# Optimization experiments

Hardware: AMD Instinct MI355X
Metric: run time of the kernel (lower is better)

## Reference

```python
import jax, jax.numpy as jnp
import numpy as np

BS, SL, WPL, NP = 32, 256, 4, 320
WD, PD, RD, HD = 768, 64, 64, 256
PN, RN, PL = 32, 64, 8
NF = 128
WINDOW_SIZES = (2, 3, 4)
FD = 2 * HD  # node feature dim


def setup_inputs() -> dict:
    key = jax.random.key(0)
    ks = jax.random.split(key, 24)
    s = 0.02
    inp = {}
    # forward tensors (bert_out stands in for BertModel output after CLS slice)
    inp["bert_out"] = jax.random.normal(ks[0], (BS, NP, WD), jnp.float32)
    inp["wordpiece_gather_idx"] = jax.random.randint(ks[1], (BS, SL, WPL), 0, NP + 1)
    inp["pos"] = jax.random.randint(ks[2], (BS, SL), 0, PN)
    inp["deprel"] = jax.random.randint(ks[3], (BS, SL), 0, RN)
    inp["path"] = jax.random.randint(ks[4], (BS, SL, PL), 0, 2 * SL + 1)
    inp["aspect_head"] = jax.random.randint(ks[5], (BS, SL), 0, SL + 1)
    inp["text_mask"] = jax.random.randint(ks[6], (BS, SL), 0, 2)
    inp["aspect_mask"] = jax.random.randint(ks[7], (BS, SL), 0, 2)
    # parameters (pad row 0 zeroed to mimic padding_idx)
    inp["pos_emb"] = (jax.random.normal(ks[8], (PN, PD)) * s).at[0].set(0.0)
    inp["deprel_emb"] = (jax.random.normal(ks[9], (RN, RD)) * s).at[0].set(0.0)
    inp["pathdepth_emb"] = (jax.random.normal(ks[10], (PL + 2, PD)) * s).at[0].set(0.0)
    inp["ext_rel"] = jax.random.normal(ks[11], (RD,)) * s
    inp["fc1_W"] = jax.random.normal(ks[12], (WD + 2 * PD, FD)) * s
    inp["fc1_b"] = jnp.zeros((FD,), jnp.float32)
    inp["bilin_W"] = jax.random.normal(ks[13], (2 * FD, RD)) * s
    inp["bilin_b"] = jnp.zeros((), jnp.float32)
    inp["W_k2"] = jax.random.normal(ks[14], (2, FD, NF)) * s
    inp["b_k2"] = jnp.zeros((NF,), jnp.float32)
    inp["W_k3"] = jax.random.normal(ks[15], (3, FD, NF)) * s
    inp["b_k3"] = jnp.zeros((NF,), jnp.float32)
    inp["W_k4"] = jax.random.normal(ks[16], (4, FD, NF)) * s
    inp["b_k4"] = jnp.zeros((NF,), jnp.float32)
    inp["fc_out_W"] = jax.random.normal(ks[17], (NF * 3, 3)) * s
    inp["fc_out_b"] = jnp.zeros((3,), jnp.float32)
    return inp


def reference(bert_out, wordpiece_gather_idx, pos, deprel, path, aspect_head,
              text_mask, aspect_mask, pos_emb, deprel_emb, pathdepth_emb, ext_rel,
              fc1_W, fc1_b, bilin_W, bilin_b,
              W_k2, b_k2, W_k3, b_k3, W_k4, b_k4, fc_out_W, fc_out_b):
    bs, sl = pos.shape
    wd = bert_out.shape[-1]
    fd = fc1_b.shape[0]
    # --- wordpiece -> word averaging (pad piece 0 is a zero vector) ---
    pieces = jnp.concatenate([jnp.zeros((bs, 1, wd), bert_out.dtype), bert_out], axis=1)  # [B, NP+1, WD]
    g = jnp.take_along_axis(pieces, wordpiece_gather_idx.reshape(bs, -1)[..., None], axis=1)
    g = g.reshape(bs, sl, -1, wd)                                   # [B, SL, WPL, WD]
    npieces = (wordpiece_gather_idx != 0).sum(-1, keepdims=True)    # [B, SL, 1]
    word = g.sum(2) / jnp.maximum(npieces, 1).astype(g.dtype)       # [B, SL, WD]
    # --- node features ---
    path_depth = (path != 0).sum(-1)                                # [B, SL]
    node_in = jnp.concatenate([word, pos_emb[pos], pathdepth_emb[path_depth]], -1)
    node = jax.nn.relu(node_in @ fc1_W + fc1_b)                     # [B, SL, FD]
    # --- edge features: gather head nodes (0 = pad word -> zeros) ---
    node_pad = jnp.concatenate([jnp.zeros((bs, 1, fd), node.dtype), node], axis=1)
    dep = jnp.take_along_axis(node_pad, aspect_head[..., None], axis=1)  # [B, SL, FD]
    head_text = jnp.concatenate([dep, node], axis=1)                # [B, 2SL, FD]
    tail_text = jnp.concatenate([node, jnp.zeros_like(node)], axis=1)
    edge = jnp.concatenate([head_text, tail_text], axis=-1)         # [B, 2SL, 2FD]
    label = jnp.concatenate([deprel_emb[deprel],
                             jnp.broadcast_to(ext_rel, (bs, sl, ext_rel.shape[0]))], axis=1)
    # bilinear score: x1^T W x2 + b, single output channel
    score = jax.nn.sigmoid(jnp.einsum('bnd,dr,bnr->bn', edge, bilin_W, label) + bilin_b)
    edge_score = jnp.concatenate([jnp.ones((bs, 1), score.dtype), score], axis=1)  # [B, 2SL+1]
    # --- node weight: product of edge scores along dependency path ---
    nw = jnp.prod(jnp.take_along_axis(edge_score[:, None, :], path, axis=2), -1)   # [B, SL]
    nw = jnp.where((text_mask != 0) & (aspect_mask == 0), nw, jnp.zeros_like(nw))
    weight_norm = nw.sum(-1)                                        # [B]
    # --- manual windowed CNN + max pool ---
    pooled = []
    for W, b in ((W_k2, b_k2), (W_k3, b_k3), (W_k4, b_k4)):
        kw = W.shape[0]
        cn = sl - kw + 1
        w_win = jnp.mean(jnp.stack([nw[:, k:k + cn] for k in range(kw)], -1), -1)  # [B, CN]
        y = sum(jnp.einsum('bnf,fm->bnm', node[:, k:k + cn, :], W[k]) for k in range(kw))
        y = w_win[..., None] * y + b                                # [B, CN, NF]
        pooled.append(y.max(axis=1))                                # [B, NF]
    sentence = jnp.concatenate(pooled, -1)
    predicts = sentence @ fc_out_W + fc_out_b                       # [B, 3]
    return predicts, weight_norm
```

## Files before the change

### kernel.cpp

```cpp
#include <hip/hip_runtime.h>
#include <hip/hip_bf16.h>
#include <math.h>

#define BSZ 32
#define SL 256
#define WPL 4
#define NP 320
#define WD 768
#define PD 64
#define RD 64
#define FD 512
#define PL 8
#define NF 128
#define NIN 896
#define ES_STRIDE 513
#define MROWS (BSZ * SL)
#define NZ 384
#define KZ 2048

typedef __attribute__((ext_vector_type(8))) short bf16x8;
typedef __attribute__((ext_vector_type(4))) float f32x4;
typedef unsigned short ushort_t;
typedef __attribute__((ext_vector_type(4))) ushort_t u16x4;

__device__ __forceinline__ ushort_t f2bf(float x) {
    __hip_bfloat16 h = __float2bfloat16(x);
    return *reinterpret_cast<ushort_t*>(&h);
}
__device__ __forceinline__ float bf2f(ushort_t u) {
    return __uint_as_float(((unsigned)u) << 16);
}

#define P0 65536
#define P1 (P0 + 512)
#define P2 (P1 + FD * NIN)
#define P3 (P2 + NZ * KZ)
#define P4 (P3 + 3 * FD)
#define PREP_BLOCKS (P4 / 256)
__global__ __launch_bounds__(256) void setup_kernel(
    const float* __restrict__ bert, const int* __restrict__ wgi,
    const int* __restrict__ pos, const int* __restrict__ path,
    const float* __restrict__ pos_emb, const float* __restrict__ pd_emb,
    const float* __restrict__ bilin_W, const float* __restrict__ deprel_emb,
    const float* __restrict__ ext_rel, const float* __restrict__ fc1_W,
    const float* __restrict__ W2, const float* __restrict__ W3,
    const float* __restrict__ W4,
    ushort_t* __restrict__ node_in,
    float* __restrict__ Ut, float* __restrict__ v,
    ushort_t* __restrict__ Wt1, ushort_t* __restrict__ WzT,
    ushort_t* __restrict__ node)
{
    const int tid = threadIdx.x;
    if (blockIdx.x < MROWS) {
        const int bs = blockIdx.x;
        const int b = bs >> 8;
        const int* gi = wgi + (size_t)bs * WPL;
        const int i0 = gi[0], i1 = gi[1], i2 = gi[2], i3 = gi[3];
        const int npc = (i0 != 0) + (i1 != 0) + (i2 != 0) + (i3 != 0);
        const float inv = 1.0f / (float)(npc > 1 ? npc : 1);
        ushort_t* out = node_in + (size_t)bs * NIN;
        if (tid < 192) {
            const float4* r0 = (const float4*)(bert + ((size_t)b * NP + (i0 - 1)) * WD);
            const float4* r1 = (const float4*)(bert + ((size_t)b * NP + (i1 - 1)) * WD);
            const float4* r2 = (const float4*)(bert + ((size_t)b * NP + (i2 - 1)) * WD);
            const float4* r3 = (const float4*)(bert + ((size_t)b * NP + (i3 - 1)) * WD);
            float4 s = make_float4(0.f, 0.f, 0.f, 0.f);
            if (i0) { float4 t = r0[tid]; s.x += t.x; s.y += t.y; s.z += t.z; s.w += t.w; }
            if (i1) { float4 t = r1[tid]; s.x += t.x; s.y += t.y; s.z += t.z; s.w += t.w; }
            if (i2) { float4 t = r2[tid]; s.x += t.x; s.y += t.y; s.z += t.z; s.w += t.w; }
            if (i3) { float4 t = r3[tid]; s.x += t.x; s.y += t.y; s.z += t.z; s.w += t.w; }
            u16x4 o;
            o[0] = f2bf(s.x * inv); o[1] = f2bf(s.y * inv);
            o[2] = f2bf(s.z * inv); o[3] = f2bf(s.w * inv);
            *reinterpret_cast<u16x4*>(&out[tid * 4]) = o;
        } else {
            const int e = tid - 192;
            out[WD + e] = f2bf(pos_emb[pos[bs] * PD + e]);
            const int* pp = path + (size_t)bs * PL;
            int pd = 0;
#pragma unroll
            for (int l = 0; l < PL; ++l) pd += (pp[l] != 0);
            out[WD + PD + e] = f2bf(pd_emb[pd * PD + e]);
        }
        return;
    }
    const int idx = (blockIdx.x - MROWS) * 256 + tid;
    if (idx < P0) {
        const int r = idx >> 10, d = idx & 1023;
        float s = 0.f;
#pragma unroll
        for (int j = 0; j < RD; ++j) s += bilin_W[d * RD + j] * deprel_emb[r * RD + j];
        Ut[idx] = s;
    } else if (idx < P1) {
        const int d = idx - P0;
        float s = 0.f;
#pragma unroll
        for (int j = 0; j < RD; ++j) s += bilin_W[d * RD + j] * ext_rel[j];
        v[d] = s;
    } else if (idx < P2) {
        const int j = idx - P1;
        const int k = j >> 9, n = j & 511;
        Wt1[(size_t)n * NIN + k] = f2bf(fc1_W[(size_t)k * FD + n]);
    } else if (idx < P3) {
        const int j = idx - P2;
        const int kp = j / NZ, c = j - kp * NZ;
        const int w = c >> 7, f = c & 127;
        const int k = kp >> 9, d = kp & 511;
        const int kw = w + 2;
        float val = 0.f;
        if (k < kw) {
            const float* Wsrc = (w == 0) ? W2 : (w == 1) ? W3 : W4;
            val = Wsrc[((size_t)k * FD + d) * NF + f];
        }
        WzT[(size_t)c * KZ + kp] = f2bf(val);
    } else if (idx < P4) {
        const int j = idx - P3;
        node[(size_t)MROWS * FD + j] = 0;
    }
}

__global__ __launch_bounds__(256) void gemm_node(
    const ushort_t* __restrict__ A,
    const ushort_t* __restrict__ Bt,
    const float* __restrict__ bias,
    ushort_t* __restrict__ C)
{
    __shared__ ushort_t As[128 * 64];
    __shared__ ushort_t Bs[64 * 64];
    const int tid = threadIdx.x;
    const int wid = tid >> 6, lane = tid & 63;
    const int wr = wid >> 1, wc = wid & 1;
    const int row0 = blockIdx.y * 128, col0 = blockIdx.x * 64;
    const int lr = lane & 15, lk = lane >> 4;
    f32x4 acc[4][2] = {};
    const ushort_t* gA0 = A + (size_t)row0 * NIN;
    const ushort_t* gB0 = Bt + (size_t)col0 * NIN;
    for (int k0 = 0; k0 < NIN; k0 += 64) {
#pragma unroll
        for (int i = 0; i < 4; ++i) {
            const int c = i * 256 + (wid << 6) + lane;
            const int r = c >> 3, q = (c & 7) ^ (r & 7);
            __builtin_amdgcn_global_load_lds(
                (const __attribute__((address_space(1))) void*)(gA0 + (size_t)r * NIN + k0 + q * 8),
                (__attribute__((address_space(3))) void*)((char*)As + i * 4096 + (wid << 10)),
                16, 0, 0);
        }
#pragma unroll
        for (int i = 0; i < 2; ++i) {
            const int c = i * 256 + (wid << 6) + lane;
            const int r = c >> 3, q = (c & 7) ^ (r & 7);
            __builtin_amdgcn_global_load_lds(
                (const __attribute__((address_space(1))) void*)(gB0 + (size_t)r * NIN + k0 + q * 8),
                (__attribute__((address_space(3))) void*)((char*)Bs + i * 4096 + (wid << 10)),
                16, 0, 0);
        }
        __syncthreads();
        bf16x8 af[4][2], bfv[2][2];
#pragma unroll
        for (int m = 0; m < 4; ++m) {
            const int fr = wr * 64 + m * 16 + lr;
#pragma unroll
            for (int ks = 0; ks < 2; ++ks)
                af[m][ks] = *reinterpret_cast<const bf16x8*>(
                    &As[fr * 64 + ((((ks << 2) | lk) ^ (fr & 7)) << 3)]);
        }
#pragma unroll
        for (int n = 0; n < 2; ++n) {
            const int fr = wc * 32 + n * 16 + lr;
#pragma unroll
            for (int ks = 0; ks < 2; ++ks)
                bfv[n][ks] = *reinterpret_cast<const bf16x8*>(
                    &Bs[fr * 64 + ((((ks << 2) | lk) ^ (fr & 7)) << 3)]);
        }
#pragma unroll
        for (int ks = 0; ks < 2; ++ks)
#pragma unroll
            for (int m = 0; m < 4; ++m)
#pragma unroll
                for (int n = 0; n < 2; ++n)
                    acc[m][n] = __builtin_amdgcn_mfma_f32_16x16x32_bf16(
                        af[m][ks], bfv[n][ks], acc[m][n], 0, 0, 0);
        __syncthreads();
    }
#pragma unroll
    for (int n = 0; n < 2; ++n) {
        const int col = col0 + wc * 32 + n * 16 + lr;
        const float bv = bias[col];
#pragma unroll
        for (int m = 0; m < 4; ++m) {
            const int rb = row0 + wr * 64 + m * 16 + lk * 4;
            const f32x4 vv = acc[m][n];
#pragma unroll
            for (int j = 0; j < 4; ++j)
                C[(size_t)(rb + j) * FD + col] = f2bf(fmaxf(vv[j] + bv, 0.f));
        }
    }
}

__global__ __launch_bounds__(256) void gemm_z_pool(
    const ushort_t* __restrict__ node,
    const ushort_t* __restrict__ WzT,
    const float* __restrict__ nw,
    const float* __restrict__ b2, const float* __restrict__ b3,
    const float* __restrict__ b4,
    float* __restrict__ pmaxp)
{
    __shared__ ushort_t As[128 * 64];
    __shared__ ushort_t Bs[64 * 64];
    const int tid = threadIdx.x;
    const int wid = tid >> 6, lane = tid & 63;
    const int wr = wid >> 1, wc = wid & 1;
    const int row0 = blockIdx.y * 128, col0 = blockIdx.x * 64;
    const int lr = lane & 15, lk = lane >> 4;
    f32x4 acc[4][2] = {};
    const ushort_t* gB0 = WzT + (size_t)col0 * KZ;
    const int Keff = ((col0 >> 7) + 2) * 512;
    for (int k0 = 0; k0 < Keff; k0 += 64) {
        const int koff = k0 >> 9;
        const int d0 = k0 & 511;
        const ushort_t* gA0 = node + (size_t)(row0 + koff) * FD + d0;
#pragma unroll
        for (int i = 0; i < 4; ++i) {
            const int c = i * 256 + (wid << 6) + lane;
            const int r = c >> 3, q = (c & 7) ^ (r & 7);
            __builtin_amdgcn_global_load_lds(
                (const __attribute__((address_space(1))) void*)(gA0 + (size_t)r * FD + q * 8),
                (__attribute__((address_space(3))) void*)((char*)As + i * 4096 + (wid << 10)),
                16, 0, 0);
        }
#pragma unroll
        for (int i = 0; i < 2; ++i) {
            const int c = i * 256 + (wid << 6) + lane;
            const int r = c >> 3, q = (c & 7) ^ (r & 7);
            __builtin_amdgcn_global_load_lds(
                (const __attribute__((address_space(1))) void*)(gB0 + (size_t)r * KZ + k0 + q * 8),
                (__attribute__((address_space(3))) void*)((char*)Bs + i * 4096 + (wid << 10)),
                16, 0, 0);
        }
        __syncthreads();
        bf16x8 af[4][2], bfv[2][2];
#pragma unroll
        for (int m = 0; m < 4; ++m) {
            const int fr = wr * 64 + m * 16 + lr;
#pragma unroll
            for (int ks = 0; ks < 2; ++ks)
                af[m][ks] = *reinterpret_cast<const bf16x8*>(
                    &As[fr * 64 + ((((ks << 2) | lk) ^ (fr & 7)) << 3)]);
        }
#pragma unroll
        for (int n = 0; n < 2; ++n) {
            const int fr = wc * 32 + n * 16 + lr;
#pragma unroll
            for (int ks = 0; ks < 2; ++ks)
                bfv[n][ks] = *reinterpret_cast<const bf16x8*>(
                    &Bs[fr * 64 + ((((ks << 2) | lk) ^ (fr & 7)) << 3)]);
        }
#pragma unroll
        for (int ks = 0; ks < 2; ++ks)
#pragma unroll
            for (int m = 0; m < 4; ++m)
#pragma unroll
                for (int n = 0; n < 2; ++n)
                    acc[m][n] = __builtin_amdgcn_mfma_f32_16x16x32_bf16(
                        af[m][ks], bfv[n][ks], acc[m][n], 0, 0, 0);
        __syncthreads();
    }
    const int bI = row0 >> 8;
    const int nn0 = row0 & 255;
    __shared__ float snw[132];
    if (tid < 132) snw[tid] = (nn0 + tid < SL) ? nw[bI * SL + nn0 + tid] : 0.f;
    __syncthreads();
    float cmax[2];
#pragma unroll
    for (int n = 0; n < 2; ++n) {
        const int col = col0 + wc * 32 + n * 16 + lr;
        const int w = col >> 7;
        const int kw = w + 2;
        const float invk = (w == 0) ? 0.5f : (w == 1) ? (1.f / 3.f) : 0.25f;
        const float bf = ((w == 0) ? b2 : (w == 1) ? b3 : b4)[col & 127];
        const int nmax = SL - kw;
        float mx = -INFINITY;
#pragma unroll
        for (int m = 0; m < 4; ++m) {
            const int rbase = wr * 64 + m * 16 + lk * 4;
            const f32x4 vv = acc[m][n];
#pragma unroll
            for (int j = 0; j < 4; ++j) {
                const int rloc = rbase + j;
                if (nn0 + rloc <= nmax) {
                    float ws = 0.f;
                    for (int k = 0; k < kw; ++k) ws += snw[rloc + k];
                    mx = fmaxf(mx, ws * invk * vv[j] + bf);
                }
            }
        }
        mx = fmaxf(mx, __shfl_xor(mx, 16));
        mx = fmaxf(mx, __shfl_xor(mx, 32));
        cmax[n] = mx;
    }
    if (lane < 16) {
#pragma unroll
        for (int n = 0; n < 2; ++n) {
            const int col = col0 + wc * 32 + n * 16 + lr;
            pmaxp[((size_t)blockIdx.y * 2 + wr) * NZ + col] = cmax[n];
        }
    }
}

__global__ __launch_bounds__(256) void score_kernel(
    const ushort_t* __restrict__ node, const int* __restrict__ aspect_head,
    const int* __restrict__ deprel, const float* __restrict__ Ut,
    const float* __restrict__ v, const float* __restrict__ bilin_b,
    float* __restrict__ edge_score)
{
    const int g = blockIdx.x * 4 + (threadIdx.x >> 6);
    const int lane = threadIdx.x & 63;
    const int b = g >> 9;
    const int n = g & 511;
    const int d0 = lane * 8;
    typedef __attribute__((ext_vector_type(8))) unsigned short u16x8;
    float sum = 0.f;
    if (n < SL) {
        const int dr = deprel[b * SL + n];
        const int h = aspect_head[b * SL + n];
        const float* uc = Ut + (size_t)dr * 1024;
        const u16x8 nv = *reinterpret_cast<const u16x8*>(&node[((size_t)b * SL + n) * FD + d0]);
        if (h != 0) {
            const u16x8 dv = *reinterpret_cast<const u16x8*>(&node[((size_t)b * SL + (h - 1)) * FD + d0]);
#pragma unroll
            for (int i = 0; i < 8; ++i) sum += bf2f(dv[i]) * uc[d0 + i];
        }
#pragma unroll
        for (int i = 0; i < 8; ++i) sum += bf2f(nv[i]) * uc[FD + d0 + i];
    } else {
        const u16x8 nv = *reinterpret_cast<const u16x8*>(&node[((size_t)b * SL + (n - SL)) * FD + d0]);
#pragma unroll
        for (int i = 0; i < 8; ++i) sum += bf2f(nv[i]) * v[d0 + i];
    }
#pragma unroll
    for (int off = 32; off > 0; off >>= 1) sum += __shfl_xor(sum, off, 64);
    if (lane == 0) {
        const float sc = 1.f / (1.f + expf(-(sum + bilin_b[0])));
        edge_score[b * ES_STRIDE + 1 + n] = sc;
        if (n == 0) edge_score[b * ES_STRIDE] = 1.0f;
    }
}

__global__ __launch_bounds__(256) void nw_kernel(
    const float* __restrict__ edge_score, const int* __restrict__ path,
    const int* __restrict__ text_mask, const int* __restrict__ aspect_mask,
    float* __restrict__ nw, float* __restrict__ weight_norm)
{
    const int b = blockIdx.x, s = threadIdx.x;
    const float* es = edge_score + b * ES_STRIDE;
    const int* pp = path + ((size_t)b * SL + s) * PL;
    float p = 1.f;
#pragma unroll
    for (int l = 0; l < PL; ++l) p *= es[pp[l]];
    if (!(text_mask[b * SL + s] != 0 && aspect_mask[b * SL + s] == 0)) p = 0.f;
    nw[b * SL + s] = p;
    __shared__ float red[256];
    red[s] = p;
    __syncthreads();
    for (int off = 128; off > 0; off >>= 1) {
        if (s < off) red[s] += red[s + off];
        __syncthreads();
    }
    if (s == 0) weight_norm[b] = red[0];
}

__global__ __launch_bounds__(384) void finish_kernel(
    const float* __restrict__ pmaxp, const float* __restrict__ W,
    const float* __restrict__ bias, float* __restrict__ out)
{
    const int b = blockIdx.x;
    const int t = threadIdx.x;
    const float* p = pmaxp + (size_t)b * 4 * NZ + t;
    float mx = -INFINITY;
#pragma unroll
    for (int i = 0; i < 4; ++i) mx = fmaxf(mx, p[(size_t)i * NZ]);
    __shared__ float sent[384];
    sent[t] = mx;
    __syncthreads();
    if (t < 3) {
        float acc = bias[t];
        for (int i = 0; i < 384; ++i) acc = fmaf(sent[i], W[i * 3 + t], acc);
        out[b * 3 + t] = acc;
    }
}

extern "C" void kernel_launch(void* const* d_in, const int* in_sizes, int n_in,
                              void* d_out, int out_size, void* d_ws, size_t ws_size,
                              hipStream_t stream)
{
    const float* bert      = (const float*)d_in[0];
    const int*   wgi       = (const int*)d_in[1];
    const int*   pos       = (const int*)d_in[2];
    const int*   deprel    = (const int*)d_in[3];
    const int*   path      = (const int*)d_in[4];
    const int*   ahead     = (const int*)d_in[5];
    const int*   tmask     = (const int*)d_in[6];
    const int*   amask     = (const int*)d_in[7];
    const float* pos_emb   = (const float*)d_in[8];
    const float* dre_emb   = (const float*)d_in[9];
    const float* pd_emb    = (const float*)d_in[10];
    const float* ext_rel   = (const float*)d_in[11];
    const float* fc1_W     = (const float*)d_in[12];
    const float* fc1_b     = (const float*)d_in[13];
    const float* bilin_W   = (const float*)d_in[14];
    const float* bilin_b   = (const float*)d_in[15];
    const float* W2        = (const float*)d_in[16];
    const float* b2        = (const float*)d_in[17];
    const float* W3        = (const float*)d_in[18];
    const float* b3        = (const float*)d_in[19];
    const float* W4        = (const float*)d_in[20];
    const float* b4        = (const float*)d_in[21];
    const float* fco_W     = (const float*)d_in[22];
    const float* fco_b     = (const float*)d_in[23];
    float* out = (float*)d_out;

    uint8_t* w = (uint8_t*)d_ws;
    ushort_t* node_in = (ushort_t*)w;
    size_t off = (size_t)MROWS * NIN * 2;
    ushort_t* node = (ushort_t*)(w + off); off += (size_t)(MROWS + 3) * FD * 2;
    ushort_t* Wt1  = (ushort_t*)(w + off); off += (size_t)FD * NIN * 2;
    ushort_t* WzT  = (ushort_t*)(w + off); off += (size_t)NZ * KZ * 2;
    float* Ut    = (float*)(w + off); off += (size_t)64 * 1024 * 4;
    float* vvec  = (float*)(w + off); off += FD * 4;
    float* es    = (float*)(w + off); off += (size_t)BSZ * ES_STRIDE * 4;
    float* nw    = (float*)(w + off); off += (size_t)BSZ * SL * 4;
    float* pmaxp = (float*)(w + off); off += (size_t)128 * NZ * 4;

    setup_kernel<<<MROWS + PREP_BLOCKS, 256, 0, stream>>>(
        bert, wgi, pos, path, pos_emb, pd_emb,
        bilin_W, dre_emb, ext_rel, fc1_W, W2, W3, W4,
        node_in, Ut, vvec, Wt1, WzT, node);

    gemm_node<<<dim3(FD / 64, MROWS / 128), 256, 0, stream>>>(node_in, Wt1, fc1_b, node);

    score_kernel<<<(BSZ * 2 * SL) / 4, 256, 0, stream>>>(
        node, ahead, deprel, Ut, vvec, bilin_b, es);

    nw_kernel<<<BSZ, 256, 0, stream>>>(es, path, tmask, amask, nw, out + 96);

    gemm_z_pool<<<dim3(NZ / 64, MROWS / 128), 256, 0, stream>>>(
        node, WzT, nw, b2, b3, b4, pmaxp);

    finish_kernel<<<BSZ, 384, 0, stream>>>(pmaxp, fco_W, fco_b, out);
}
```

Baseline: 112.3 us.

## Precompute embedding projections as bias tables and fuse score with node-weight kernel

The pos and path-depth embedding columns are no longer concatenated into the fc1 input. Their fc1 contributions, with fc1_b folded in, are precomputed into small tables (32 and 10 rows by 512) that the GEMM epilogue adds per row, so the GEMM K dimension drops from 896 to 768. Weight transposes now go through shared-memory 32x32 tiles, which gives coalesced writes. The score and nw kernels are merged into one 32-block kernel that keeps edge scores in LDS, removing a launch and a global round-trip, but this gives much less parallelism for the score computation. The epilogue also adds gathered bias loads per element.

Result: slower. 149.0 us (+32.7%).

```diff
diff --git a/kernel.cpp b/kernel.cpp
--- a/kernel.cpp
+++ b/kernel.cpp
@@ -12,7 +12,6 @@
 #define FD 512
 #define PL 8
 #define NF 128
-#define NIN 896
 #define ES_STRIDE 513
 #define MROWS (BSZ * SL)
 #define NZ 384
@@ -31,34 +30,42 @@
     return __uint_as_float(((unsigned)u) << 16);
 }
 
-#define P0 65536
-#define P1 (P0 + 512)
-#define P2 (P1 + FD * NIN)
-#define P3 (P2 + NZ * KZ)
-#define P4 (P3 + 3 * FD)
-#define PREP_BLOCKS (P4 / 256)
+#define NB_GATHER MROWS
+#define B_WW   NB_GATHER
+#define NB_WW  384
+#define B_TAB  (B_WW + NB_WW)
+#define NB_TAB 42
+#define B_WZT  (B_TAB + NB_TAB)
+#define NB_WZT 576
+#define B_PAD  (B_WZT + NB_WZT)
+#define NB_PAD 2
+#define B_UT   (B_PAD + NB_PAD)
+#define NB_UT  258
+#define NB_TOTAL (B_UT + NB_UT)
+
 __global__ __launch_bounds__(256) void setup_kernel(
     const float* __restrict__ bert, const int* __restrict__ wgi,
     const int* __restrict__ pos, const int* __restrict__ path,
     const float* __restrict__ pos_emb, const float* __restrict__ pd_emb,
     const float* __restrict__ bilin_W, const float* __restrict__ deprel_emb,
     const float* __restrict__ ext_rel, const float* __restrict__ fc1_W,
+    const float* __restrict__ fc1_b,
     const float* __restrict__ W2, const float* __restrict__ W3,
     const float* __restrict__ W4,
-    ushort_t* __restrict__ node_in,
-    float* __restrict__ Ut, float* __restrict__ v,
-    ushort_t* __restrict__ Wt1, ushort_t* __restrict__ WzT,
-    ushort_t* __restrict__ node)
+    ushort_t* __restrict__ word, int* __restrict__ depth,
+    ushort_t* __restrict__ Ww, float* __restrict__ posc, float* __restrict__ pdc,
+    ushort_t* __restrict__ WzT, ushort_t* __restrict__ node,
+    float* __restrict__ Ut, float* __restrict__ v)
 {
     const int tid = threadIdx.x;
-    if (blockIdx.x < MROWS) {
-        const int bs = blockIdx.x;
+    const int blk = blockIdx.x;
+    if (blk < NB_GATHER) {
+        const int bs = blk;
         const int b = bs >> 8;
         const int* gi = wgi + (size_t)bs * WPL;
         const int i0 = gi[0], i1 = gi[1], i2 = gi[2], i3 = gi[3];
         const int npc = (i0 != 0) + (i1 != 0) + (i2 != 0) + (i3 != 0);
         const float inv = 1.0f / (float)(npc > 1 ? npc : 1);
-        ushort_t* out = node_in + (size_t)bs * NIN;
         if (tid < 192) {
             const float4* r0 = (const float4*)(bert + ((size_t)b * NP + (i0 - 1)) * WD);
             const float4* r1 = (const float4*)(bert + ((size_t)b * NP + (i1 - 1)) * WD);
@@ -72,76 +79,132 @@
             u16x4 o;
             o[0] = f2bf(s.x * inv); o[1] = f2bf(s.y * inv);
             o[2] = f2bf(s.z * inv); o[3] = f2bf(s.w * inv);
-            *reinterpret_cast<u16x4*>(&out[tid * 4]) = o;
-        } else {
-            const int e = tid - 192;
-            out[WD + e] = f2bf(pos_emb[pos[bs] * PD + e]);
+            *reinterpret_cast<u16x4*>(&word[(size_t)bs * WD + tid * 4]) = o;
+        } else if (tid == 192) {
             const int* pp = path + (size_t)bs * PL;
             int pd = 0;
 #pragma unroll
             for (int l = 0; l < PL; ++l) pd += (pp[l] != 0);
-            out[WD + PD + e] = f2bf(pd_emb[pd * PD + e]);
+            depth[bs] = pd;
         }
         return;
     }
-    const int idx = (blockIdx.x - MROWS) * 256 + tid;
-    if (idx < P0) {
-        const int r = idx >> 10, d = idx & 1023;
-        float s = 0.f;
-#pragma unroll
-        for (int j = 0; j < RD; ++j) s += bilin_W[d * RD + j] * deprel_emb[r * RD + j];
-        Ut[idx] = s;
-    } else if (idx < P1) {
-        const int d = idx - P0;
-        float s = 0.f;
-#pragma unroll
-        for (int j = 0; j < RD; ++j) s += bilin_W[d * RD + j] * ext_rel[j];
-        v[d] = s;
-    } else if (idx < P2) {
-        const int j = idx - P1;
-        const int k = j >> 9, n = j & 511;
-        Wt1[(size_t)n * NIN + k] = f2bf(fc1_W[(size_t)k * FD + n]);
-    } else if (idx < P3) {
-        const int j = idx - P2;
-        const int kp = j / NZ, c = j - kp * NZ;
-        const int w = c >> 7, f = c & 127;
-        const int k = kp >> 9, d = kp & 511;
-        const int kw = w + 2;
-        float val = 0.f;
-        if (k < kw) {
-            const float* Wsrc = (w == 0) ? W2 : (w == 1) ? W3 : W4;
-            val = Wsrc[((size_t)k * FD + d) * NF + f];
-        }
-        WzT[(size_t)c * KZ + kp] = f2bf(val);
-    } else if (idx < P4) {
-        const int j = idx - P3;
-        node[(size_t)MROWS * FD + j] = 0;
+    if (blk < B_TAB) {
+        __shared__ float s[32][33];
+        const int t = blk - B_WW;
+        const int kt = t % 24, nt = t / 24;
+#pragma unroll
+        for (int i = 0; i < 4; ++i) {
+            const int idx = i * 256 + tid;
+            const int kk = idx >> 5, nn = idx & 31;
+            s[kk][nn] = fc1_W[(size_t)(kt * 32 + kk) * FD + nt * 32 + nn];
+        }
+        __syncthreads();
+#pragma unroll
+        for (int i = 0; i < 4; ++i) {
+            const int idx = i * 256 + tid;
+            const int nn = idx >> 5, kk = idx & 31;
+            Ww[(size_t)(nt * 32 + nn) * WD + kt * 32 + kk] = f2bf(s[kk][nn]);
+        }
+        return;
+    }
+    if (blk < B_WZT) {
+        const int r = blk - B_TAB;
+#pragma unroll
+        for (int h = 0; h < 2; ++h) {
+            const int cc = tid + h * 256;
+            if (r < 32) {
+                float acc = fc1_b[cc];
+#pragma unroll
+                for (int j = 0; j < PD; ++j)
+                    acc += pos_emb[r * PD + j] * fc1_W[(size_t)(WD + j) * FD + cc];
+                posc[(size_t)r * FD + cc] = acc;
+            } else {
+                const int r2 = r - 32;
+                float acc = 0.f;
+#pragma unroll
+                for (int j = 0; j < PD; ++j)
+                    acc += pd_emb[r2 * PD + j] * fc1_W[(size_t)(WD + PD + j) * FD + cc];
+                pdc[(size_t)r2 * FD + cc] = acc;
+            }
+        }
+        return;
+    }
+    if (blk < B_PAD) {
+        __shared__ float s[32][33];
+        const int t2 = blk - B_WZT;
+        const int p = t2 / 64, tt = t2 % 64;
+        const int dt = tt & 15, ft = tt >> 4;
+        int w, k; const float* src;
+        if (p < 2)      { w = 0; k = p;     src = W2; }
+        else if (p < 5) { w = 1; k = p - 2; src = W3; }
+        else            { w = 2; k = p - 5; src = W4; }
+#pragma unroll
+        for (int i = 0; i < 4; ++i) {
+            const int idx = i * 256 + tid;
+            const int dd = idx >> 5, ff = idx & 31;
+            s[dd][ff] = src[((size_t)k * FD + dt * 32 + dd) * NF + ft * 32 + ff];
+        }
+        __syncthreads();
+#pragma unroll
+        for (int i = 0; i < 4; ++i) {
+            const int idx = i * 256 + tid;
+            const int ff = idx >> 5, dd = idx & 31;
+            WzT[(size_t)(w * NF + ft * 32 + ff) * KZ + k * FD + dt * 32 + dd] = f2bf(s[dd][ff]);
+        }
+        return;
+    }
+    if (blk < B_UT) {
+        const int local = (blk - B_PAD) * 256 + tid;
+#pragma unroll
+        for (int j = 0; j < 3; ++j) node[(size_t)MROWS * FD + local * 3 + j] = 0;
+        return;
+    }
+    {
+        const int idx = (blk - B_UT) * 256 + tid;
+        if (idx < 65536) {
+            const int r = idx >> 10, d = idx & 1023;
+            float s = 0.f;
+#pragma unroll
+            for (int j = 0; j < RD; ++j) s += bilin_W[d * RD + j] * deprel_emb[r * RD + j];
+            Ut[idx] = s;
+        } else if (idx < 65536 + FD) {
+            const int d = idx - 65536;
+            float s = 0.f;
+#pragma unroll
+            for (int j = 0; j < RD; ++j) s += bilin_W[d * RD + j] * ext_rel[j];
+            v[d] = s;
+        }
+        return;
     }
 }
 
 __global__ __launch_bounds__(256) void gemm_node(
     const ushort_t* __restrict__ A,
     const ushort_t* __restrict__ Bt,
-    const float* __restrict__ bias,
+    const int* __restrict__ pos, const int* __restrict__ depth,
+    const float* __restrict__ posc, const float* __restrict__ pdc,
     ushort_t* __restrict__ C)
 {
     __shared__ ushort_t As[128 * 64];
     __shared__ ushort_t Bs[64 * 64];
+    __shared__ int spos[128], sdep[128];
     const int tid = threadIdx.x;
     const int wid = tid >> 6, lane = tid & 63;
     const int wr = wid >> 1, wc = wid & 1;
     const int row0 = blockIdx.y * 128, col0 = blockIdx.x * 64;
     const int lr = lane & 15, lk = lane >> 4;
+    if (tid < 128) { spos[tid] = pos[row0 + tid]; sdep[tid] = depth[row0 + tid]; }
     f32x4 acc[4][2] = {};
-    const ushort_t* gA0 = A + (size_t)row0 * NIN;
-    const ushort_t* gB0 = Bt + (size_t)col0 * NIN;
-    for (int k0 = 0; k0 < NIN; k0 += 64) {
+    const ushort_t* gA0 = A + (size_t)row0 * WD;
+    const ushort_t* gB0 = Bt + (size_t)col0 * WD;
+    for (int k0 = 0; k0 < WD; k0 += 64) {
 #pragma unroll
         for (int i = 0; i < 4; ++i) {
             const int c = i * 256 + (wid << 6) + lane;
             const int r = c >> 3, q = (c & 7) ^ (r & 7);
             __builtin_amdgcn_global_load_lds(
-                (const __attribute__((address_space(1))) void*)(gA0 + (size_t)r * NIN + k0 + q * 8),
+                (const __attribute__((address_space(1))) void*)(gA0 + (size_t)r * WD + k0 + q * 8),
                 (__attribute__((address_space(3))) void*)((char*)As + i * 4096 + (wid << 10)),
                 16, 0, 0);
         }
@@ -150,7 +213,7 @@
             const int c = i * 256 + (wid << 6) + lane;
             const int r = c >> 3, q = (c & 7) ^ (r & 7);
             __builtin_amdgcn_global_load_lds(
-                (const __attribute__((address_space(1))) void*)(gB0 + (size_t)r * NIN + k0 + q * 8),
+                (const __attribute__((address_space(1))) void*)(gB0 + (size_t)r * WD + k0 + q * 8),
                 (__attribute__((address_space(3))) void*)((char*)Bs + i * 4096 + (wid << 10)),
                 16, 0, 0);
         }
@@ -185,16 +248,77 @@
 #pragma unroll
     for (int n = 0; n < 2; ++n) {
         const int col = col0 + wc * 32 + n * 16 + lr;
-        const float bv = bias[col];
 #pragma unroll
         for (int m = 0; m < 4; ++m) {
-            const int rb = row0 + wr * 64 + m * 16 + lk * 4;
             const f32x4 vv = acc[m][n];
 #pragma unroll
-            for (int j = 0; j < 4; ++j)
-                C[(size_t)(rb + j) * FD + col] = f2bf(fmaxf(vv[j] + bv, 0.f));
-        }
-    }
+            for (int j = 0; j < 4; ++j) {
+                const int rloc = wr * 64 + m * 16 + lk * 4 + j;
+                const float bv = posc[(size_t)spos[rloc] * FD + col]
+                               + pdc[(size_t)sdep[rloc] * FD + col];
+                C[(size_t)(row0 + rloc) * FD + col] = f2bf(fmaxf(vv[j] + bv, 0.f));
+            }
+        }
+    }
+}
+
+__global__ __launch_bounds__(512) void score_nw_kernel(
+    const ushort_t* __restrict__ node, const int* __restrict__ aspect_head,
+    const int* __restrict__ deprel, const float* __restrict__ Ut,
+    const float* __restrict__ v, const float* __restrict__ bilin_b,
+    const int* __restrict__ path, const int* __restrict__ text_mask,
+    const int* __restrict__ aspect_mask,
+    float* __restrict__ nw, float* __restrict__ weight_norm)
+{
+    __shared__ float es[ES_STRIDE];
+    __shared__ float red[256];
+    const int b = blockIdx.x;
+    const int tid = threadIdx.x;
+    const int wv = tid >> 6, lane = tid & 63;
+    const int d0 = lane * 8;
+    const float bb = bilin_b[0];
+    typedef __attribute__((ext_vector_type(8))) unsigned short u16x8;
+    if (tid == 0) es[0] = 1.0f;
+    for (int e = wv; e < 2 * SL; e += 8) {
+        float sum = 0.f;
+        if (e < SL) {
+            const int dr = deprel[b * SL + e];
+            const int h = aspect_head[b * SL + e];
+            const float* uc = Ut + (size_t)dr * 1024;
+            const u16x8 nv = *reinterpret_cast<const u16x8*>(&node[((size_t)b * SL + e) * FD + d0]);
+            if (h != 0) {
+                const u16x8 dv = *reinterpret_cast<const u16x8*>(&node[((size_t)b * SL + (h - 1)) * FD + d0]);
+#pragma unroll
+                for (int i = 0; i < 8; ++i) sum += bf2f(dv[i]) * uc[d0 + i];
+            }
+#pragma unroll
+            for (int i = 0; i < 8; ++i) sum += bf2f(nv[i]) * uc[FD + d0 + i];
+        } else {
+            const u16x8 nv = *reinterpret_cast<const u16x8*>(&node[((size_t)b * SL + (e - SL)) * FD + d0]);
+#pragma unroll
+            for (int i = 0; i < 8; ++i) sum += bf2f(nv[i]) * v[d0 + i];
+        }
+#pragma unroll
+        for (int off = 32; off > 0; off >>= 1) sum += __shfl_xor(sum, off, 64);
+        if (lane == 0) es[1 + e] = 1.f / (1.f + expf(-(sum + bb)));
+    }
+    __syncthreads();
+    if (tid < 256) {
+        const int s = tid;
+        const int* pp = path + ((size_t)b * SL + s) * PL;
+        float p = 1.f;
+#pragma unroll
+        for (int l = 0; l < PL; ++l) p *= es[pp[l]];
+        if (!(text_mask[b * SL + s] != 0 && aspect_mask[b * SL + s] == 0)) p = 0.f;
+        nw[b * SL + s] = p;
+        red[s] = p;
+    }
+    __syncthreads();
+    for (int off = 128; off > 0; off >>= 1) {
+        if (tid < off) red[tid] += red[tid + off];
+        __syncthreads();
+    }
+    if (tid == 0) weight_norm[b] = red[0];
 }
 
 __global__ __launch_bounds__(256) void gemm_z_pool(
@@ -305,68 +429,6 @@
             pmaxp[((size_t)blockIdx.y * 2 + wr) * NZ + col] = cmax[n];
         }
     }
-}
-
-__global__ __launch_bounds__(256) void score_kernel(
-    const ushort_t* __restrict__ node, const int* __restrict__ aspect_head,
-    const int* __restrict__ deprel, const float* __restrict__ Ut,
-    const float* __restrict__ v, const float* __restrict__ bilin_b,
-    float* __restrict__ edge_score)
-{
-    const int g = blockIdx.x * 4 + (threadIdx.x >> 6);
-    const int lane = threadIdx.x & 63;
-    const int b = g >> 9;
-    const int n = g & 511;
-    const int d0 = lane * 8;
-    typedef __attribute__((ext_vector_type(8))) unsigned short u16x8;
-    float sum = 0.f;
-    if (n < SL) {
-        const int dr = deprel[b * SL + n];
-        const int h = aspect_head[b * SL + n];
-        const float* uc = Ut + (size_t)dr * 1024;
-        const u16x8 nv = *reinterpret_cast<const u16x8*>(&node[((size_t)b * SL + n) * FD + d0]);
-        if (h != 0) {
-            const u16x8 dv = *reinterpret_cast<const u16x8*>(&node[((size_t)b * SL + (h - 1)) * FD + d0]);
-#pragma unroll
-            for (int i = 0; i < 8; ++i) sum += bf2f(dv[i]) * uc[d0 + i];
-        }
-#pragma unroll
-        for (int i = 0; i < 8; ++i) sum += bf2f(nv[i]) * uc[FD + d0 + i];
-    } else {
-        const u16x8 nv = *reinterpret_cast<const u16x8*>(&node[((size_t)b * SL + (n - SL)) * FD + d0]);
-#pragma unroll
-        for (int i = 0; i < 8; ++i) sum += bf2f(nv[i]) * v[d0 + i];
-    }
-#pragma unroll
-    for (int off = 32; off > 0; off >>= 1) sum += __shfl_xor(sum, off, 64);
-    if (lane == 0) {
-        const float sc = 1.f / (1.f + expf(-(sum + bilin_b[0])));
-        edge_score[b * ES_STRIDE + 1 + n] = sc;
-        if (n == 0) edge_score[b * ES_STRIDE] = 1.0f;
-    }
-}
-
-__global__ __launch_bounds__(256) void nw_kernel(
-    const float* __restrict__ edge_score, const int* __restrict__ path,
-    const int* __restrict__ text_mask, const int* __restrict__ aspect_mask,
-    float* __restrict__ nw, float* __restrict__ weight_norm)
-{
-    const int b = blockIdx.x, s = threadIdx.x;
-    const float* es = edge_score + b * ES_STRIDE;
-    const int* pp = path + ((size_t)b * SL + s) * PL;
-    float p = 1.f;
-#pragma unroll
-    for (int l = 0; l < PL; ++l) p *= es[pp[l]];
-    if (!(text_mask[b * SL + s] != 0 && aspect_mask[b * SL + s] == 0)) p = 0.f;
-    nw[b * SL + s] = p;
-    __shared__ float red[256];
-    red[s] = p;
-    __syncthreads();
-    for (int off = 128; off > 0; off >>= 1) {
-        if (s < off) red[s] += red[s + off];
-        __syncthreads();
-    }
-    if (s == 0) weight_norm[b] = red[0];
 }
 
 __global__ __launch_bounds__(384) void finish_kernel(
@@ -420,28 +482,29 @@
     float* out = (float*)d_out;
 
     uint8_t* w = (uint8_t*)d_ws;
-    ushort_t* node_in = (ushort_t*)w;
-    size_t off = (size_t)MROWS * NIN * 2;
+    size_t off = 0;
+    ushort_t* word = (ushort_t*)(w + off); off += (size_t)MROWS * WD * 2;
     ushort_t* node = (ushort_t*)(w + off); off += (size_t)(MROWS + 3) * FD * 2;
-    ushort_t* Wt1  = (ushort_t*)(w + off); off += (size_t)FD * NIN * 2;
+    ushort_t* Ww   = (ushort_t*)(w + off); off += (size_t)FD * WD * 2;
     ushort_t* WzT  = (ushort_t*)(w + off); off += (size_t)NZ * KZ * 2;
     float* Ut    = (float*)(w + off); off += (size_t)64 * 1024 * 4;
     float* vvec  = (float*)(w + off); off += FD * 4;
-    float* es    = (float*)(w + off); off += (size_t)BSZ * ES_STRIDE * 4;
+    float* posc  = (float*)(w + off); off += (size_t)32 * FD * 4;
+    float* pdc   = (float*)(w + off); off += (size_t)10 * FD * 4;
     float* nw    = (float*)(w + off); off += (size_t)BSZ * SL * 4;
     float* pmaxp = (float*)(w + off); off += (size_t)128 * NZ * 4;
-
-    setup_kernel<<<MROWS + PREP_BLOCKS, 256, 0, stream>>>(
+    int*   depth = (int*)(w + off);  off += (size_t)MROWS * 4;
+
+    setup_kernel<<<NB_TOTAL, 256, 0, stream>>>(
         bert, wgi, pos, path, pos_emb, pd_emb,
-        bilin_W, dre_emb, ext_rel, fc1_W, W2, W3, W4,
-        node_in, Ut, vvec, Wt1, WzT, node);
-
-    gemm_node<<<dim3(FD / 64, MROWS / 128), 256, 0, stream>>>(node_in, Wt1, fc1_b, node);
-
-    score_kernel<<<(BSZ * 2 * SL) / 4, 256, 0, stream>>>(
-        node, ahead, deprel, Ut, vvec, bilin_b, es);
-
-    nw_kernel<<<BSZ, 256, 0, stream>>>(es, path, tmask, amask, nw, out + 96);
+        bilin_W, dre_emb, ext_rel, fc1_W, fc1_b, W2, W3, W4,
+        word, depth, Ww, posc, pdc, WzT, node, Ut, vvec);
+
+    gemm_node<<<dim3(FD / 64, MROWS / 128), 256, 0, stream>>>(
+        word, Ww, pos, depth, posc, pdc, node);
+
+    score_nw_kernel<<<BSZ, 512, 0, stream>>>(
+        node, ahead, deprel, Ut, vvec, bilin_b, path, tmask, amask, nw, out + 96);
 
     gemm_z_pool<<<dim3(NZ / 64, MROWS / 128), 256, 0, stream>>>(
         node, WzT, nw, b2, b3, b4, pmaxp);
```
